# Kernel optimization log

Hardware: AMD Instinct MI355X
Metric: run time of the kernel (lower is better)

## Reference

```python
import jax, jax.numpy as jnp
import numpy as np

OFFSET = (0, 0)
STRIDE = (2, 2)

B, C, H, W = 2, 256, 384, 384
N_ACTIVE = 16384
GRID = 192  # strided index grid: OFFSET + (GRID-1)*STRIDE < H


def setup_inputs() -> dict:
    key = jax.random.key(0)
    k1, k2, k3 = jax.random.split(key, 3)
    x = jax.random.normal(k1, (B, C, N_ACTIVE), dtype=jnp.float32)
    original_output = jax.random.normal(k2, (B, C, H, W), dtype=jnp.float32)
    active_indices = jax.random.randint(k3, (N_ACTIVE, 2), 0, GRID, dtype=jnp.int32)
    return {"x": x, "original_output": original_output, "active_indices": active_indices}


def reference(x, original_output, active_indices):
    # Scatter-write active values into the dense output at strided/offset coords.
    # write location for active index k: (OFFSET[0] + iy*STRIDE[0], OFFSET[1] + ix*STRIDE[1])
    h = OFFSET[0] + active_indices[:, 0] * STRIDE[0]  # [N]
    w = OFFSET[1] + active_indices[:, 1] * STRIDE[1]  # [N]
    # advanced indexing on the two spatial dims -> [B, C, N] slots, overwritten by x
    out = original_output.at[:, :, h, w].set(x)
    return out
```

## Files before the change

### kernel.cpp

```cpp
#include <hip/hip_runtime.h>

#define BB      2
#define CC      256
#define HH      384
#define WW      384
#define N_ACT   16384
#define GRID_N  192
#define PLANE_F4 ((HH * WW) / 4)
#define ROW_F4   (WW / 4)
#define PAIRS_PER_PLANE (PLANE_F4 / 2)

typedef float  fx4 __attribute__((ext_vector_type(4)));

__global__ void winner_scatter_kernel(const int2* __restrict__ idx,
                                      int* __restrict__ winner) {
    int k = blockIdx.x * blockDim.x + threadIdx.x;
    if (k < N_ACT) {
        int2 p = idx[k];
        atomicMax(&winner[p.x * GRID_N + p.y], k);
    }
}

__global__ void scatter_main_kernel(const fx4* __restrict__ orig,
                                    const float* __restrict__ x,
                                    const int* __restrict__ winner,
                                    fx4* __restrict__ out) {
    int bc = blockIdx.y;
    int q  = blockIdx.x * blockDim.x + threadIdx.x;
    int gy  = q / ROW_F4;
    int col = q - gy * ROW_F4;

    int base = bc * PLANE_F4 + (gy * 2) * ROW_F4 + col;

    const int2* wrow2 = reinterpret_cast<const int2*>(winner + gy * GRID_N);
    int2 w = wrow2[col];
    fx4 ve = __builtin_nontemporal_load(&orig[base]);
    fx4 vo = __builtin_nontemporal_load(&orig[base + ROW_F4]);

    if (w.x >= 0 || w.y >= 0) {
        const float* xp = x + bc * N_ACT;
        if (w.x >= 0) ve[0] = xp[w.x];
        if (w.y >= 0) ve[2] = xp[w.y];
    }

    out[base] = ve;
    out[base + ROW_F4] = vo;
}

extern "C" void kernel_launch(void* const* d_in, const int* in_sizes, int n_in,
                              void* d_out, int out_size, void* d_ws, size_t ws_size,
                              hipStream_t stream) {
    const float* x    = (const float*)d_in[0];
    const float* orig = (const float*)d_in[1];
    const int*   idx  = (const int*)d_in[2];
    float*       out  = (float*)d_out;
    int*         winner = (int*)d_ws;

    (void)hipMemsetAsync(winner, 0xFF, GRID_N * GRID_N * sizeof(int), stream);
    winner_scatter_kernel<<<dim3((N_ACT + 255) / 256), dim3(256), 0, stream>>>(
        (const int2*)idx, winner);
    scatter_main_kernel<<<dim3(PAIRS_PER_PLANE / 256, BB * CC), dim3(256), 0, stream>>>(
        (const fx4*)orig, x, winner, (fx4*)out);
}
```

Baseline: 138.4 us.

## Compact winning x values in cell order via scan so gathers become coalesced

```diff
diff --git a/kernel.cpp b/kernel.cpp
--- a/kernel.cpp
+++ b/kernel.cpp
@@ -6,11 +6,14 @@
 #define WW      384
 #define N_ACT   16384
 #define GRID_N  192
+#define NCELL   (GRID_N * GRID_N)
 #define PLANE_F4 ((HH * WW) / 4)
 #define ROW_F4   (WW / 4)
 #define PAIRS_PER_PLANE (PLANE_F4 / 2)
+#define SCAN_T  1024
+#define CPT     (NCELL / SCAN_T)
 
-typedef float  fx4 __attribute__((ext_vector_type(4)));
+typedef float fx4 __attribute__((ext_vector_type(4)));
 
 __global__ void winner_scatter_kernel(const int2* __restrict__ idx,
                                       int* __restrict__ winner) {
@@ -21,9 +24,51 @@
     }
 }
 
+__global__ void __launch_bounds__(SCAN_T)
+scan_kernel(const int* __restrict__ winner, int* __restrict__ packed) {
+    __shared__ int s[SCAN_T];
+    int t = threadIdx.x;
+    int base = t * CPT;
+
+    int w[CPT];
+    int cnt = 0;
+#pragma unroll
+    for (int i = 0; i < CPT; ++i) {
+        w[i] = winner[base + i];
+        cnt += (w[i] >= 0);
+    }
+    s[t] = cnt;
+    __syncthreads();
+    for (int off = 1; off < SCAN_T; off <<= 1) {
+        int v = (t >= off) ? s[t - off] : 0;
+        __syncthreads();
+        s[t] += v;
+        __syncthreads();
+    }
+    int rank = s[t] - cnt;
+#pragma unroll
+    for (int i = 0; i < CPT; ++i) {
+        int wi = w[i];
+        packed[base + i] = (wi >= 0) ? ((wi << 16) | rank) : -1;
+        rank += (wi >= 0);
+    }
+}
+
+__global__ void build_xs_kernel(const float* __restrict__ x,
+                                const int2* __restrict__ idx,
+                                const int* __restrict__ packed,
+                                float* __restrict__ xs) {
+    int bc = blockIdx.y;
+    int k  = blockIdx.x * blockDim.x + threadIdx.x;
+    int2 p = idx[k];
+    int pk = packed[p.x * GRID_N + p.y];
+    if (pk != -1 && (pk >> 16) == k)
+        xs[bc * N_ACT + (pk & 0xFFFF)] = x[bc * N_ACT + k];
+}
+
 __global__ void scatter_main_kernel(const fx4* __restrict__ orig,
-                                    const float* __restrict__ x,
-                                    const int* __restrict__ winner,
+                                    const float* __restrict__ xs,
+                                    const int* __restrict__ packed,
                                     fx4* __restrict__ out) {
     int bc = blockIdx.y;
     int q  = blockIdx.x * blockDim.x + threadIdx.x;
@@ -32,16 +77,14 @@
 
     int base = bc * PLANE_F4 + (gy * 2) * ROW_F4 + col;
 
-    const int2* wrow2 = reinterpret_cast<const int2*>(winner + gy * GRID_N);
-    int2 w = wrow2[col];
+    const int2* prow2 = reinterpret_cast<const int2*>(packed + gy * GRID_N);
+    int2 pk = prow2[col];
     fx4 ve = __builtin_nontemporal_load(&orig[base]);
     fx4 vo = __builtin_nontemporal_load(&orig[base + ROW_F4]);
 
-    if (w.x >= 0 || w.y >= 0) {
-        const float* xp = x + bc * N_ACT;
-        if (w.x >= 0) ve[0] = xp[w.x];
-        if (w.y >= 0) ve[2] = xp[w.y];
-    }
+    const float* xsp = xs + bc * N_ACT;
+    if (pk.x != -1) ve[0] = xsp[pk.x & 0xFFFF];
+    if (pk.y != -1) ve[2] = xsp[pk.y & 0xFFFF];
 
     out[base] = ve;
     out[base + ROW_F4] = vo;
@@ -54,11 +97,18 @@
     const float* orig = (const float*)d_in[1];
     const int*   idx  = (const int*)d_in[2];
     float*       out  = (float*)d_out;
-    int*         winner = (int*)d_ws;
 
-    (void)hipMemsetAsync(winner, 0xFF, GRID_N * GRID_N * sizeof(int), stream);
+    char* ws = (char*)d_ws;
+    int*   winner = (int*)ws;
+    int*   packed = (int*)(ws + NCELL * 4);
+    float* xs     = (float*)(ws + 2 * NCELL * 4);
+
+    (void)hipMemsetAsync(winner, 0xFF, NCELL * sizeof(int), stream);
     winner_scatter_kernel<<<dim3((N_ACT + 255) / 256), dim3(256), 0, stream>>>(
         (const int2*)idx, winner);
+    scan_kernel<<<dim3(1), dim3(SCAN_T), 0, stream>>>(winner, packed);
+    build_xs_kernel<<<dim3(N_ACT / 256, BB * CC), dim3(256), 0, stream>>>(
+        x, (const int2*)idx, packed, xs);
     scatter_main_kernel<<<dim3(PAIRS_PER_PLANE / 256, BB * CC), dim3(256), 0, stream>>>(
-        (const fx4*)orig, x, winner, (fx4*)out);
+        (const fx4*)orig, xs, packed, (fx4*)out);
 }
```

Result: slower. 230.6 us (+66.6%).
